# Kernel optimization log

Measured on AMD Instinct MI355X. Metric: run time of the kernel, lower is better.

Reference implementation:

```python
import jax, jax.numpy as jnp
import numpy as np

VAR_CXCY = 0.1   # variances[0]
VAR_WH = 0.2     # variances[1]
MIN_OVERLAP = 0.5
NEG_POS_RATIO = 3


def cxcy_to_xyxy(b):
    return jnp.concatenate([b[:, :2] - b[:, 2:] / 2, b[:, :2] + b[:, 2:] / 2], axis=-1)


def jaccard(a, b):
    # a: [O,4] xyxy, b: [P,4] xyxy -> [O,P]
    lt = jnp.maximum(a[:, None, :2], b[None, :, :2])
    rb = jnp.minimum(a[:, None, 2:], b[None, :, 2:])
    wh = jnp.clip(rb - lt, 0.0)
    inter = wh[..., 0] * wh[..., 1]
    area_a = (a[:, 2] - a[:, 0]) * (a[:, 3] - a[:, 1])
    area_b = (b[:, 2] - b[:, 0]) * (b[:, 3] - b[:, 1])
    return inter / (area_a[:, None] + area_b[None, :] - inter)


def xyxy_to_gcxgcy(boxes, priors):
    # boxes: [P,4] xyxy matched per-prior; priors: [P,4] cxcywh
    cxcy = (boxes[:, :2] + boxes[:, 2:]) / 2
    wh = boxes[:, 2:] - boxes[:, :2]
    g_cxcy = (cxcy - priors[:, :2]) / (priors[:, 2:] * VAR_CXCY)
    g_wh = jnp.log(wh / priors[:, 2:]) / VAR_WH
    return jnp.concatenate([g_cxcy, g_wh], axis=-1)


def _match_one(boxes, labels, priors, priors_xyxy):
    # boxes: [O,4] xyxy, labels: [O] int
    overlaps = jaccard(boxes, priors_xyxy)          # [O,P]
    prior_overlaps = overlaps.max(axis=0)            # [P]
    prior_objects = overlaps.argmax(axis=0)          # [P]
    object_priors = overlaps.argmax(axis=1)          # [O] best prior per object
    n_obj = boxes.shape[0]
    prior_objects = prior_objects.at[object_priors].set(jnp.arange(n_obj))
    prior_overlaps = prior_overlaps.at[object_priors].set(1.0)
    lab = labels[prior_objects]
    lab = jnp.where(prior_overlaps < MIN_OVERLAP, 0, lab)
    locs = xyxy_to_gcxgcy(boxes[prior_objects], priors)
    return locs, lab


def setup_inputs() -> dict:
    key = jax.random.key(0)
    B, P, C, O = 64, 8732, 81, 16
    ks = jax.random.split(key, 6)
    predict_locs = jax.random.normal(ks[0], (B, P, 4), dtype=jnp.float32)
    predict_confs = jax.random.normal(ks[1], (B, P, C), dtype=jnp.float32)
    # priors in cxcywh, valid sizes
    p_cxcy = jax.random.uniform(ks[2], (P, 2), minval=0.0, maxval=1.0)
    p_wh = jax.random.uniform(ks[2], (P, 2), minval=0.05, maxval=0.3)
    priors = jnp.concatenate([p_cxcy, p_wh], axis=-1).astype(jnp.float32)
    # targets: valid xyxy boxes in [0,1]
    t_cxcy = jax.random.uniform(ks[3], (B, O, 2), minval=0.2, maxval=0.8)
    t_wh = jax.random.uniform(ks[4], (B, O, 2), minval=0.05, maxval=0.4)
    target_boxes = jnp.concatenate([t_cxcy - t_wh / 2, t_cxcy + t_wh / 2], axis=-1).astype(jnp.float32)
    target_labels = jax.random.randint(ks[5], (B, O), 1, C)
    return {
        'predict_locs': predict_locs,
        'predict_confs': predict_confs,
        'target_boxes': target_boxes,
        'target_labels': target_labels,
        'priors': priors,
    }


def reference(predict_locs, predict_confs, target_boxes, target_labels, priors):
    priors_xyxy = cxcy_to_xyxy(priors)
    true_locs, true_confs = jax.vmap(
        lambda b, l: _match_one(b, l, priors, priors_xyxy)
    )(target_boxes, target_labels)              # [B,P,4], [B,P]

    pos = true_confs != 0                        # [B,P]
    n_pos = pos.sum(axis=1)                      # [B]
    n_pos_total = n_pos.sum().astype(predict_locs.dtype)

    # nn.L1Loss(reduction='mean') over the [n_pos_total, 4] gathered entries
    loc_loss = jnp.sum(jnp.abs(predict_locs - true_locs) * pos[..., None]) / (n_pos_total * 4)

    logp = jax.nn.log_softmax(predict_confs, axis=-1)
    ce = -jnp.take_along_axis(logp, true_confs[..., None], axis=-1)[..., 0]  # [B,P]

    ce_pos_sum = jnp.sum(jnp.where(pos, ce, 0.0))
    ce_neg = jnp.where(pos, 0.0, ce)
    # double-sort rank: rank of each prior when sorted by descending neg loss
    rank = jnp.argsort(jnp.argsort(-ce_neg, axis=1), axis=1)
    hard = rank < (NEG_POS_RATIO * n_pos)[:, None]
    ce_hard_sum = jnp.sum(jnp.where(hard, ce_neg, 0.0))

    conf_loss = (ce_hard_sum + ce_pos_sum) / n_pos_total
    return conf_loss + loc_loss
```

## Files before the change

kernel.cpp:

```cpp
#include <hip/hip_runtime.h>
#include <cstdint>
#include <cstddef>

constexpr int O_C = 16;
constexpr int P_MAX = 8732;
constexpr int CH   = 4;
constexpr int CHP  = 2183;

__device__ __forceinline__ float waveSumF(float v) {
    #pragma unroll
    for (int off = 32; off; off >>= 1) v += __shfl_xor(v, off);
    return v;
}
__device__ __forceinline__ int waveSumI(int v) {
    #pragma unroll
    for (int off = 32; off; off >>= 1) v += __shfl_xor(v, off);
    return v;
}

__global__ __launch_bounds__(256) void matchA1(
    const float* __restrict__ target_boxes,
    const float* __restrict__ priors,
    float* __restrict__ ov_out,
    unsigned char* __restrict__ obj_out,
    unsigned long long* __restrict__ okey_part,
    int P)
{
    const int b    = blockIdx.x / CH;
    const int c    = blockIdx.x % CH;
    const int tid  = threadIdx.x;
    const int lane = tid & 63;
    const int wid  = tid >> 6;

    __shared__ float bx0[O_C], by0[O_C], bx1[O_C], by1[O_C], barea[O_C];
    __shared__ unsigned long long s_wb[O_C * 4];

    if (tid < O_C) {
        const float* tb = target_boxes + ((size_t)b * O_C + tid) * 4;
        float x0 = tb[0], y0 = tb[1], x1 = tb[2], y1 = tb[3];
        bx0[tid] = x0; by0[tid] = y0; bx1[tid] = x1; by1[tid] = y1;
        barea[tid] = (x1 - x0) * (y1 - y0);
    }
    __syncthreads();

    float bi[O_C]; int bp[O_C];
    #pragma unroll
    for (int o = 0; o < O_C; ++o) { bi[o] = -1.0f; bp[o] = 0; }

    const int p0 = c * CHP, p1 = min(p0 + CHP, P);
    for (int p = p0 + tid; p < p1; p += 256) {
        float4 pr = reinterpret_cast<const float4*>(priors)[p];
        float px0 = pr.x - pr.z * 0.5f, py0 = pr.y - pr.w * 0.5f;
        float px1 = pr.x + pr.z * 0.5f, py1 = pr.y + pr.w * 0.5f;
        float parea = (px1 - px0) * (py1 - py0);
        float bv = -1.0f; int bo = 0;
        #pragma unroll
        for (int o = 0; o < O_C; ++o) {
            float ix0 = fmaxf(px0, bx0[o]), iy0 = fmaxf(py0, by0[o]);
            float ix1 = fminf(px1, bx1[o]), iy1 = fminf(py1, by1[o]);
            float iw = fmaxf(ix1 - ix0, 0.0f), ih = fmaxf(iy1 - iy0, 0.0f);
            float inter = iw * ih;
            float iou = inter / (barea[o] + parea - inter);
            if (iou > bv) { bv = iou; bo = o; }
            if (iou > bi[o]) { bi[o] = iou; bp[o] = p; }
        }
        ov_out[(size_t)b * P + p]  = bv;
        obj_out[(size_t)b * P + p] = (unsigned char)bo;
    }

    #pragma unroll
    for (int o = 0; o < O_C; ++o) {
        unsigned long long k = (bi[o] >= 0.0f)
            ? (((unsigned long long)__float_as_uint(bi[o]) << 32) |
               (unsigned long long)(0xFFFFFFFFu - (unsigned)bp[o]))
            : 0ull;
        #pragma unroll
        for (int off = 32; off; off >>= 1) {
            unsigned long long k2 = __shfl_xor(k, off);
            if (k2 > k) k = k2;
        }
        if (lane == 0) s_wb[o * 4 + wid] = k;
    }
    __syncthreads();
    if (tid < O_C) {
        unsigned long long k = s_wb[tid * 4];
        #pragma unroll
        for (int w = 1; w < 4; ++w) if (s_wb[tid * 4 + w] > k) k = s_wb[tid * 4 + w];
        okey_part[(size_t)blockIdx.x * O_C + tid] = k;
    }
}

__global__ __launch_bounds__(256) void fused_ce(
    const float* __restrict__ confs,
    const float* __restrict__ ov_in,
    const unsigned char* __restrict__ obj_in,
    const unsigned long long* __restrict__ okey_part,
    const float* __restrict__ target_boxes,
    const int*   __restrict__ target_labels,
    const float* __restrict__ priors,
    const float* __restrict__ predict_locs,
    float* __restrict__ ce_out,
    float* __restrict__ loc_part,
    int P, int rows)
{
    constexpr int C = 81;
    constexpr int R = 64;
    __shared__ float s_x[R * C];
    __shared__ float tbx0[2][O_C], tby0[2][O_C], tbx1[2][O_C], tby1[2][O_C];
    __shared__ int   tlab[2][O_C], toprior[2][O_C];
    __shared__ float s_facc[4];

    const int tid  = threadIdx.x;
    const int lane = tid & 63;
    const int wid  = tid >> 6;
    const int row0 = blockIdx.x * R;

    const int b0     = row0 / P;
    const int rsplit = min(row0 + R, (b0 + 1) * P);
    const bool two   = rsplit < row0 + R;
    const int b1     = two ? b0 + 1 : b0;

    if (tid < 2 * O_C) {
        const int seg = tid >> 4, o = tid & 15;
        const int bb  = seg ? b1 : b0;
        const float* tb = target_boxes + ((size_t)bb * O_C + o) * 4;
        tbx0[seg][o] = tb[0]; tby0[seg][o] = tb[1];
        tbx1[seg][o] = tb[2]; tby1[seg][o] = tb[3];
        tlab[seg][o] = target_labels[(size_t)bb * O_C + o];
        unsigned long long k = 0ull;
        #pragma unroll
        for (int c = 0; c < CH; ++c) {
            unsigned long long k2 = okey_part[((size_t)bb * CH + c) * O_C + o];
            if (k2 > k) k = k2;
        }
        toprior[seg][o] = (int)(0xFFFFFFFFu - (unsigned)(k & 0xFFFFFFFFull));
    }

    {
        const float4* src = reinterpret_cast<const float4*>(confs + (size_t)row0 * C);
        float4* dst = reinterpret_cast<float4*>(s_x);
        const int nv = (R * C) / 4;
        for (int i = tid; i < nv; i += 256) dst[i] = src[i];
    }
    __syncthreads();

    const int rl = tid >> 2;
    const int q  = tid & 3;
    const int s  = q * 20 + (q > 0 ? 1 : 0);
    const int n  = q ? 20 : 21;
    const float* xr = s_x + rl * C;
    const int row = row0 + rl;

    int   l = 0;
    float locacc = 0.0f;
    if (q == 0 && row < rows) {
        const int seg = (row >= rsplit) ? 1 : 0;
        const int p   = row - (seg ? b1 : b0) * P;
        float ov = ov_in[row];
        int  obj = obj_in[row];
        #pragma unroll
        for (int o = 0; o < O_C; ++o) {
            if (toprior[seg][o] == p) { obj = o; ov = 1.0f; }
        }
        l = (ov < 0.5f) ? 0 : tlab[seg][obj];
        if (l != 0) {
            float4 pr = reinterpret_cast<const float4*>(priors)[p];
            float x0 = tbx0[seg][obj], y0 = tby0[seg][obj];
            float x1 = tbx1[seg][obj], y1 = tby1[seg][obj];
            float cx = (x0 + x1) * 0.5f, cy = (y0 + y1) * 0.5f;
            float w  = x1 - x0,          h  = y1 - y0;
            float g0 = (cx - pr.x) / (pr.z * 0.1f);
            float g1 = (cy - pr.y) / (pr.w * 0.1f);
            float g2 = logf(w / pr.z) / 0.2f;
            float g3 = logf(h / pr.w) / 0.2f;
            float4 pl = reinterpret_cast<const float4*>(predict_locs)[row];
            locacc = fabsf(pl.x - g0) + fabsf(pl.y - g1) +
                     fabsf(pl.z - g2) + fabsf(pl.w - g3);
        }
    }

    float v[21];
    #pragma unroll
    for (int i = 0; i < 21; ++i)
        v[i] = (i < n) ? xr[s + i] : -3.0e38f;

    float m = v[0];
    #pragma unroll
    for (int i = 1; i < 21; ++i) m = fmaxf(m, v[i]);
    m = fmaxf(m, __shfl_xor(m, 1));
    m = fmaxf(m, __shfl_xor(m, 2));

    float sum = 0.0f;
    #pragma unroll
    for (int i = 0; i < 21; ++i)
        if (i < n) sum += __expf(v[i] - m);
    sum += __shfl_xor(sum, 1);
    sum += __shfl_xor(sum, 2);

    if (q == 0 && row < rows) {
        float cev = m + __logf(sum) - xr[l];
        ce_out[row] = (l != 0) ? -cev : cev;
    }

    float a = waveSumF(locacc);
    if (lane == 0) s_facc[wid] = a;
    __syncthreads();
    if (tid == 0)
        loc_part[blockIdx.x] = s_facc[0] + s_facc[1] + s_facc[2] + s_facc[3];
}

__global__ __launch_bounds__(1024) void hard_kernel(
    const float* __restrict__ ce,
    int*   __restrict__ n_pos,
    float* __restrict__ ce_pos,
    float* __restrict__ ce_hard,
    int P)
{
    const int b    = blockIdx.x;
    const int tid  = threadIdx.x;
    const int lane = tid & 63;
    const int wid  = tid >> 6;

    __shared__ float s_v[P_MAX];
    __shared__ unsigned int hist[16][256];
    __shared__ unsigned int s_sel;
    __shared__ int s_kr;
    __shared__ float s_f[16], s_f2[16];
    __shared__ int s_i[16];

    const size_t base = (size_t)b * P;
    float possum = 0.0f, negsum = 0.0f;
    int cnt = 0;
    for (int p = tid; p < P; p += 1024) {
        float c = ce[base + p];
        unsigned u = __float_as_uint(c);
        float sv;
        if (u >> 31) { possum += -c; ++cnt; sv = 0.0f; }
        else         { negsum += c;         sv = c;    }
        s_v[p] = sv;
    }
    possum = waveSumF(possum);
    negsum = waveSumF(negsum);
    cnt    = waveSumI(cnt);
    if (lane == 0) { s_f[wid] = possum; s_f2[wid] = negsum; s_i[wid] = cnt; }
    __syncthreads();
    float negsum_t = 0.0f, possum_t = 0.0f; int np = 0;
    #pragma unroll
    for (int w = 0; w < 16; ++w) { negsum_t += s_f2[w]; possum_t += s_f[w]; np += s_i[w]; }
    if (tid == 0) { ce_pos[b] = possum_t; n_pos[b] = np; }

    const int K = 3 * np;
    if (K <= 0) { if (tid == 0) ce_hard[b] = 0.0f; return; }
    if (K >= P) { if (tid == 0) ce_hard[b] = negsum_t; return; }

    unsigned int prefix = 0; int kr = K;
    for (int shift = 24; shift >= 0; shift -= 8) {
        for (int i = tid; i < 16 * 256; i += 1024) (&hist[0][0])[i] = 0;
        __syncthreads();
        unsigned int maskHi = (shift == 24) ? 0u : (0xFFFFFFFFu << (shift + 8));
        for (int p = tid; p < P; p += 1024) {
            unsigned int u = __float_as_uint(s_v[p]);
            if ((u & maskHi) == prefix) atomicAdd(&hist[wid][(u >> shift) & 255], 1u);
        }
        __syncthreads();
        if (wid == 0) {
            unsigned h0 = 0, h1 = 0, h2 = 0, h3 = 0;
            #pragma unroll 4
            for (int w = 0; w < 16; ++w) {
                h0 += hist[w][lane * 4 + 0];
                h1 += hist[w][lane * 4 + 1];
                h2 += hist[w][lane * 4 + 2];
                h3 += hist[w][lane * 4 + 3];
            }
            unsigned own = h0 + h1 + h2 + h3;
            unsigned t = own;
            #pragma unroll
            for (int off = 1; off < 64; off <<= 1) {
                unsigned u = __shfl_down(t, off);
                if (lane + off >= 64) u = 0;
                t += u;
            }
            unsigned Tnext = t - own;
            unsigned cum3 = Tnext;
            unsigned cum2 = cum3 + h3;
            unsigned cum1 = cum2 + h2;
            unsigned cum0 = cum1 + h1;
            unsigned kru = (unsigned)kr;
            int selj = -1; unsigned cg = 0;
            if      (cum3 < kru && kru <= cum3 + h3) { selj = 3; cg = cum3; }
            else if (cum2 < kru && kru <= cum2 + h2) { selj = 2; cg = cum2; }
            else if (cum1 < kru && kru <= cum1 + h1) { selj = 1; cg = cum1; }
            else if (cum0 < kru && kru <= cum0 + h0) { selj = 0; cg = cum0; }
            if (selj >= 0) {
                s_sel = prefix | ((unsigned)(lane * 4 + selj) << shift);
                s_kr  = kr - (int)cg;
            }
        }
        __syncthreads();
        prefix = s_sel; kr = s_kr;
        __syncthreads();
    }

    float sumgt = 0.0f;
    for (int p = tid; p < P; p += 1024) {
        unsigned int u = __float_as_uint(s_v[p]);
        if (u > prefix) sumgt += s_v[p];
    }
    sumgt = waveSumF(sumgt);
    if (lane == 0) s_f[wid] = sumgt;
    __syncthreads();
    if (tid == 0) {
        float sg = 0.0f;
        #pragma unroll
        for (int w = 0; w < 16; ++w) sg += s_f[w];
        ce_hard[b] = sg + (float)kr * __uint_as_float(prefix);
    }
}

__global__ __launch_bounds__(256) void finalize_kernel(
    const int*   __restrict__ n_pos,
    const float* __restrict__ ce_pos,
    const float* __restrict__ ce_hard,
    const float* __restrict__ loc_part,
    float* __restrict__ out, int B, int nblk)
{
    __shared__ float s_f[4];
    __shared__ float s_res[3];
    const int tid  = threadIdx.x;
    const int lane = tid & 63;
    const int wid  = tid >> 6;

    float la = 0.0f;
    for (int i = tid; i < nblk; i += 256) la += loc_part[i];
    la = waveSumF(la);
    if (lane == 0) s_f[wid] = la;

    if (tid < 64) {
        int np = 0; float cp = 0.0f, ch = 0.0f;
        for (int b = lane; b < B; b += 64) {
            np += n_pos[b]; cp += ce_pos[b]; ch += ce_hard[b];
        }
        #pragma unroll
        for (int off = 32; off; off >>= 1) {
            np += __shfl_xor(np, off);
            cp += __shfl_xor(cp, off);
            ch += __shfl_xor(ch, off);
        }
        if (lane == 0) {
            s_res[0] = (float)np; s_res[1] = cp; s_res[2] = ch;
        }
    }
    __syncthreads();
    if (tid == 0) {
        float latot = s_f[0] + s_f[1] + s_f[2] + s_f[3];
        float npt = s_res[0];
        out[0] = (s_res[2] + s_res[1]) / npt + latot / (npt * 4.0f);
    }
}

extern "C" void kernel_launch(void* const* d_in, const int* in_sizes, int n_in,
                              void* d_out, int out_size, void* d_ws, size_t ws_size,
                              hipStream_t stream) {
    const float* predict_locs  = (const float*)d_in[0];
    const float* predict_confs = (const float*)d_in[1];
    const float* target_boxes  = (const float*)d_in[2];
    const int*   target_labels = (const int*)d_in[3];
    const float* priors        = (const float*)d_in[4];

    const int P = in_sizes[4] / 4;
    const int B = in_sizes[0] / (P * 4);
    const int rows = B * P;
    const int nblk = (rows + 63) / 64;

    char* ws = (char*)d_ws;
    unsigned long long* okey_part = (unsigned long long*)ws;
    ws += (size_t)B * CH * O_C * sizeof(unsigned long long);
    float* ce      = (float*)ws; ws += (size_t)rows * sizeof(float);
    float* ov      = (float*)ws; ws += (size_t)rows * sizeof(float);
    float* loc_p   = (float*)ws; ws += (size_t)nblk * sizeof(float);
    int*   n_pos   = (int*)ws;   ws += (size_t)B * sizeof(int);
    float* ce_pos  = (float*)ws; ws += (size_t)B * sizeof(float);
    float* ce_hard = (float*)ws; ws += (size_t)B * sizeof(float);
    unsigned char* obj = (unsigned char*)ws; ws += (size_t)rows;

    matchA1<<<B * CH, 256, 0, stream>>>(target_boxes, priors, ov, obj, okey_part, P);
    fused_ce<<<nblk, 256, 0, stream>>>(predict_confs, ov, obj, okey_part,
                                       target_boxes, target_labels, priors,
                                       predict_locs, ce, loc_p, P, rows);
    hard_kernel<<<B, 1024, 0, stream>>>(ce, n_pos, ce_pos, ce_hard, P);
    finalize_kernel<<<1, 256, 0, stream>>>(n_pos, ce_pos, ce_hard, loc_p,
                                           (float*)d_out, B, nblk);
}
```

Baseline: 89.20 us.

## Merge four kernels into one persistent cooperative kernel with grid syncs

Replaces the match, CE, hard-mining and finalize launches with a single cooperative kernel of 256 blocks of 1024 threads, separated by grid-wide syncs. The CE stage is now a persistent tile loop that register-prefetches the next confidence tile into a double-buffered shared slot. The aim is to remove launch gaps and tail effects between the small kernels. In exchange it adds grid-barrier cost, uses far fewer and larger blocks with one block per CU, and the union of shared buffers may limit occupancy.

```diff
diff --git a/kernel.cpp b/kernel.cpp
--- a/kernel.cpp
+++ b/kernel.cpp
@@ -1,11 +1,18 @@
 #include <hip/hip_runtime.h>
+#include <hip/hip_cooperative_groups.h>
 #include <cstdint>
 #include <cstddef>
 
-constexpr int O_C = 16;
+namespace cg = cooperative_groups;
+
+constexpr int O_C   = 16;
+constexpr int CH    = 4;
+constexpr int CHP   = 2183;
 constexpr int P_MAX = 8732;
-constexpr int CH   = 4;
-constexpr int CHP  = 2183;
+constexpr int NBLK  = 256;
+constexpr int NTHR  = 1024;
+constexpr int RT    = 64;
+constexpr int TV4   = RT * 81 / 4;
 
 __device__ __forceinline__ float waveSumF(float v) {
     #pragma unroll
@@ -18,343 +25,366 @@
     return v;
 }
 
-__global__ __launch_bounds__(256) void matchA1(
-    const float* __restrict__ target_boxes,
-    const float* __restrict__ priors,
-    float* __restrict__ ov_out,
-    unsigned char* __restrict__ obj_out,
-    unsigned long long* __restrict__ okey_part,
-    int P)
-{
-    const int b    = blockIdx.x / CH;
-    const int c    = blockIdx.x % CH;
-    const int tid  = threadIdx.x;
-    const int lane = tid & 63;
-    const int wid  = tid >> 6;
-
-    __shared__ float bx0[O_C], by0[O_C], bx1[O_C], by1[O_C], barea[O_C];
-    __shared__ unsigned long long s_wb[O_C * 4];
-
-    if (tid < O_C) {
-        const float* tb = target_boxes + ((size_t)b * O_C + tid) * 4;
-        float x0 = tb[0], y0 = tb[1], x1 = tb[2], y1 = tb[3];
-        bx0[tid] = x0; by0[tid] = y0; bx1[tid] = x1; by1[tid] = y1;
-        barea[tid] = (x1 - x0) * (y1 - y0);
-    }
-    __syncthreads();
-
-    float bi[O_C]; int bp[O_C];
-    #pragma unroll
-    for (int o = 0; o < O_C; ++o) { bi[o] = -1.0f; bp[o] = 0; }
-
-    const int p0 = c * CHP, p1 = min(p0 + CHP, P);
-    for (int p = p0 + tid; p < p1; p += 256) {
-        float4 pr = reinterpret_cast<const float4*>(priors)[p];
-        float px0 = pr.x - pr.z * 0.5f, py0 = pr.y - pr.w * 0.5f;
-        float px1 = pr.x + pr.z * 0.5f, py1 = pr.y + pr.w * 0.5f;
-        float parea = (px1 - px0) * (py1 - py0);
-        float bv = -1.0f; int bo = 0;
-        #pragma unroll
-        for (int o = 0; o < O_C; ++o) {
-            float ix0 = fmaxf(px0, bx0[o]), iy0 = fmaxf(py0, by0[o]);
-            float ix1 = fminf(px1, bx1[o]), iy1 = fminf(py1, by1[o]);
-            float iw = fmaxf(ix1 - ix0, 0.0f), ih = fmaxf(iy1 - iy0, 0.0f);
-            float inter = iw * ih;
-            float iou = inter / (barea[o] + parea - inter);
-            if (iou > bv) { bv = iou; bo = o; }
-            if (iou > bi[o]) { bi[o] = iou; bp[o] = p; }
-        }
-        ov_out[(size_t)b * P + p]  = bv;
-        obj_out[(size_t)b * P + p] = (unsigned char)bo;
-    }
-
-    #pragma unroll
-    for (int o = 0; o < O_C; ++o) {
-        unsigned long long k = (bi[o] >= 0.0f)
-            ? (((unsigned long long)__float_as_uint(bi[o]) << 32) |
-               (unsigned long long)(0xFFFFFFFFu - (unsigned)bp[o]))
-            : 0ull;
-        #pragma unroll
-        for (int off = 32; off; off >>= 1) {
-            unsigned long long k2 = __shfl_xor(k, off);
-            if (k2 > k) k = k2;
-        }
-        if (lane == 0) s_wb[o * 4 + wid] = k;
-    }
-    __syncthreads();
-    if (tid < O_C) {
-        unsigned long long k = s_wb[tid * 4];
-        #pragma unroll
-        for (int w = 1; w < 4; ++w) if (s_wb[tid * 4 + w] > k) k = s_wb[tid * 4 + w];
-        okey_part[(size_t)blockIdx.x * O_C + tid] = k;
-    }
-}
-
-__global__ __launch_bounds__(256) void fused_ce(
+__global__ __launch_bounds__(NTHR, 1) void mbloss_coop(
     const float* __restrict__ confs,
-    const float* __restrict__ ov_in,
-    const unsigned char* __restrict__ obj_in,
-    const unsigned long long* __restrict__ okey_part,
     const float* __restrict__ target_boxes,
     const int*   __restrict__ target_labels,
     const float* __restrict__ priors,
     const float* __restrict__ predict_locs,
-    float* __restrict__ ce_out,
-    float* __restrict__ loc_part,
-    int P, int rows)
+    float* __restrict__ ov_g,
+    unsigned char* __restrict__ obj_g,
+    unsigned long long* __restrict__ okey_part,
+    float* __restrict__ ce_g,
+    float* __restrict__ locsum_g,
+    int*   __restrict__ n_pos_g,
+    float* __restrict__ ce_pos_g,
+    float* __restrict__ ce_hard_g,
+    float* __restrict__ out,
+    int P, int B, int rows)
 {
-    constexpr int C = 81;
-    constexpr int R = 64;
-    __shared__ float s_x[R * C];
-    __shared__ float tbx0[2][O_C], tby0[2][O_C], tbx1[2][O_C], tby1[2][O_C];
-    __shared__ int   tlab[2][O_C], toprior[2][O_C];
-    __shared__ float s_facc[4];
-
+    cg::grid_group grid = cg::this_grid();
+    const int bid  = blockIdx.x;
     const int tid  = threadIdx.x;
     const int lane = tid & 63;
     const int wid  = tid >> 6;
-    const int row0 = blockIdx.x * R;
-
-    const int b0     = row0 / P;
-    const int rsplit = min(row0 + R, (b0 + 1) * P);
-    const bool two   = rsplit < row0 + R;
-    const int b1     = two ? b0 + 1 : b0;
-
-    if (tid < 2 * O_C) {
-        const int seg = tid >> 4, o = tid & 15;
-        const int bb  = seg ? b1 : b0;
-        const float* tb = target_boxes + ((size_t)bb * O_C + o) * 4;
-        tbx0[seg][o] = tb[0]; tby0[seg][o] = tb[1];
-        tbx1[seg][o] = tb[2]; tby1[seg][o] = tb[3];
-        tlab[seg][o] = target_labels[(size_t)bb * O_C + o];
-        unsigned long long k = 0ull;
+
+    __shared__ union {
+        float x[2][RT * 81];
+        struct { float v[P_MAX]; unsigned int hist[16][256]; } h;
+    } u;
+    __shared__ float4 tbox[2][2][O_C];
+    __shared__ int    ttlab[2][2][O_C], ttopr[2][2][O_C];
+    __shared__ unsigned long long s_wb[O_C][16];
+    __shared__ float s_mb[5][O_C];
+    __shared__ float s_f[16], s_f2[16];
+    __shared__ int   s_i[16];
+    __shared__ unsigned int s_sel;
+    __shared__ int s_kr;
+
+    for (int chunk = bid; chunk < B * CH; chunk += NBLK) {
+        const int b = chunk / CH, c = chunk % CH;
+        if (tid < O_C) {
+            const float* tb = target_boxes + ((size_t)b * O_C + tid) * 4;
+            float x0 = tb[0], y0 = tb[1], x1 = tb[2], y1 = tb[3];
+            s_mb[0][tid] = x0; s_mb[1][tid] = y0;
+            s_mb[2][tid] = x1; s_mb[3][tid] = y1;
+            s_mb[4][tid] = (x1 - x0) * (y1 - y0);
+        }
+        __syncthreads();
+
+        float bi[O_C]; int bp[O_C];
         #pragma unroll
-        for (int c = 0; c < CH; ++c) {
-            unsigned long long k2 = okey_part[((size_t)bb * CH + c) * O_C + o];
-            if (k2 > k) k = k2;
-        }
-        toprior[seg][o] = (int)(0xFFFFFFFFu - (unsigned)(k & 0xFFFFFFFFull));
-    }
-
-    {
-        const float4* src = reinterpret_cast<const float4*>(confs + (size_t)row0 * C);
-        float4* dst = reinterpret_cast<float4*>(s_x);
-        const int nv = (R * C) / 4;
-        for (int i = tid; i < nv; i += 256) dst[i] = src[i];
-    }
-    __syncthreads();
-
-    const int rl = tid >> 2;
-    const int q  = tid & 3;
-    const int s  = q * 20 + (q > 0 ? 1 : 0);
-    const int n  = q ? 20 : 21;
-    const float* xr = s_x + rl * C;
-    const int row = row0 + rl;
-
-    int   l = 0;
-    float locacc = 0.0f;
-    if (q == 0 && row < rows) {
-        const int seg = (row >= rsplit) ? 1 : 0;
-        const int p   = row - (seg ? b1 : b0) * P;
-        float ov = ov_in[row];
-        int  obj = obj_in[row];
+        for (int o = 0; o < O_C; ++o) { bi[o] = -1.0f; bp[o] = 0; }
+
+        const int p0 = c * CHP, p1 = min(p0 + CHP, P);
+        for (int p = p0 + tid; p < p1; p += NTHR) {
+            float4 pr = reinterpret_cast<const float4*>(priors)[p];
+            float px0 = pr.x - pr.z * 0.5f, py0 = pr.y - pr.w * 0.5f;
+            float px1 = pr.x + pr.z * 0.5f, py1 = pr.y + pr.w * 0.5f;
+            float parea = (px1 - px0) * (py1 - py0);
+            float bv = -1.0f; int bo = 0;
+            #pragma unroll
+            for (int o = 0; o < O_C; ++o) {
+                float ix0 = fmaxf(px0, s_mb[0][o]), iy0 = fmaxf(py0, s_mb[1][o]);
+                float ix1 = fminf(px1, s_mb[2][o]), iy1 = fminf(py1, s_mb[3][o]);
+                float iw = fmaxf(ix1 - ix0, 0.0f), ih = fmaxf(iy1 - iy0, 0.0f);
+                float inter = iw * ih;
+                float iou = inter / (s_mb[4][o] + parea - inter);
+                if (iou > bv) { bv = iou; bo = o; }
+                if (iou > bi[o]) { bi[o] = iou; bp[o] = p; }
+            }
+            ov_g[(size_t)b * P + p]  = bv;
+            obj_g[(size_t)b * P + p] = (unsigned char)bo;
+        }
+
         #pragma unroll
         for (int o = 0; o < O_C; ++o) {
-            if (toprior[seg][o] == p) { obj = o; ov = 1.0f; }
-        }
-        l = (ov < 0.5f) ? 0 : tlab[seg][obj];
-        if (l != 0) {
-            float4 pr = reinterpret_cast<const float4*>(priors)[p];
-            float x0 = tbx0[seg][obj], y0 = tby0[seg][obj];
-            float x1 = tbx1[seg][obj], y1 = tby1[seg][obj];
-            float cx = (x0 + x1) * 0.5f, cy = (y0 + y1) * 0.5f;
-            float w  = x1 - x0,          h  = y1 - y0;
-            float g0 = (cx - pr.x) / (pr.z * 0.1f);
-            float g1 = (cy - pr.y) / (pr.w * 0.1f);
-            float g2 = logf(w / pr.z) / 0.2f;
-            float g3 = logf(h / pr.w) / 0.2f;
-            float4 pl = reinterpret_cast<const float4*>(predict_locs)[row];
-            locacc = fabsf(pl.x - g0) + fabsf(pl.y - g1) +
-                     fabsf(pl.z - g2) + fabsf(pl.w - g3);
-        }
-    }
-
-    float v[21];
-    #pragma unroll
-    for (int i = 0; i < 21; ++i)
-        v[i] = (i < n) ? xr[s + i] : -3.0e38f;
-
-    float m = v[0];
-    #pragma unroll
-    for (int i = 1; i < 21; ++i) m = fmaxf(m, v[i]);
-    m = fmaxf(m, __shfl_xor(m, 1));
-    m = fmaxf(m, __shfl_xor(m, 2));
-
-    float sum = 0.0f;
-    #pragma unroll
-    for (int i = 0; i < 21; ++i)
-        if (i < n) sum += __expf(v[i] - m);
-    sum += __shfl_xor(sum, 1);
-    sum += __shfl_xor(sum, 2);
-
-    if (q == 0 && row < rows) {
-        float cev = m + __logf(sum) - xr[l];
-        ce_out[row] = (l != 0) ? -cev : cev;
-    }
-
-    float a = waveSumF(locacc);
-    if (lane == 0) s_facc[wid] = a;
-    __syncthreads();
-    if (tid == 0)
-        loc_part[blockIdx.x] = s_facc[0] + s_facc[1] + s_facc[2] + s_facc[3];
-}
-
-__global__ __launch_bounds__(1024) void hard_kernel(
-    const float* __restrict__ ce,
-    int*   __restrict__ n_pos,
-    float* __restrict__ ce_pos,
-    float* __restrict__ ce_hard,
-    int P)
-{
-    const int b    = blockIdx.x;
-    const int tid  = threadIdx.x;
-    const int lane = tid & 63;
-    const int wid  = tid >> 6;
-
-    __shared__ float s_v[P_MAX];
-    __shared__ unsigned int hist[16][256];
-    __shared__ unsigned int s_sel;
-    __shared__ int s_kr;
-    __shared__ float s_f[16], s_f2[16];
-    __shared__ int s_i[16];
-
-    const size_t base = (size_t)b * P;
-    float possum = 0.0f, negsum = 0.0f;
-    int cnt = 0;
-    for (int p = tid; p < P; p += 1024) {
-        float c = ce[base + p];
-        unsigned u = __float_as_uint(c);
-        float sv;
-        if (u >> 31) { possum += -c; ++cnt; sv = 0.0f; }
-        else         { negsum += c;         sv = c;    }
-        s_v[p] = sv;
-    }
-    possum = waveSumF(possum);
-    negsum = waveSumF(negsum);
-    cnt    = waveSumI(cnt);
-    if (lane == 0) { s_f[wid] = possum; s_f2[wid] = negsum; s_i[wid] = cnt; }
-    __syncthreads();
-    float negsum_t = 0.0f, possum_t = 0.0f; int np = 0;
-    #pragma unroll
-    for (int w = 0; w < 16; ++w) { negsum_t += s_f2[w]; possum_t += s_f[w]; np += s_i[w]; }
-    if (tid == 0) { ce_pos[b] = possum_t; n_pos[b] = np; }
-
-    const int K = 3 * np;
-    if (K <= 0) { if (tid == 0) ce_hard[b] = 0.0f; return; }
-    if (K >= P) { if (tid == 0) ce_hard[b] = negsum_t; return; }
-
-    unsigned int prefix = 0; int kr = K;
-    for (int shift = 24; shift >= 0; shift -= 8) {
-        for (int i = tid; i < 16 * 256; i += 1024) (&hist[0][0])[i] = 0;
-        __syncthreads();
-        unsigned int maskHi = (shift == 24) ? 0u : (0xFFFFFFFFu << (shift + 8));
-        for (int p = tid; p < P; p += 1024) {
-            unsigned int u = __float_as_uint(s_v[p]);
-            if ((u & maskHi) == prefix) atomicAdd(&hist[wid][(u >> shift) & 255], 1u);
-        }
-        __syncthreads();
-        if (wid == 0) {
-            unsigned h0 = 0, h1 = 0, h2 = 0, h3 = 0;
-            #pragma unroll 4
-            for (int w = 0; w < 16; ++w) {
-                h0 += hist[w][lane * 4 + 0];
-                h1 += hist[w][lane * 4 + 1];
-                h2 += hist[w][lane * 4 + 2];
-                h3 += hist[w][lane * 4 + 3];
-            }
-            unsigned own = h0 + h1 + h2 + h3;
-            unsigned t = own;
-            #pragma unroll
-            for (int off = 1; off < 64; off <<= 1) {
-                unsigned u = __shfl_down(t, off);
-                if (lane + off >= 64) u = 0;
-                t += u;
-            }
-            unsigned Tnext = t - own;
-            unsigned cum3 = Tnext;
-            unsigned cum2 = cum3 + h3;
-            unsigned cum1 = cum2 + h2;
-            unsigned cum0 = cum1 + h1;
-            unsigned kru = (unsigned)kr;
-            int selj = -1; unsigned cg = 0;
-            if      (cum3 < kru && kru <= cum3 + h3) { selj = 3; cg = cum3; }
-            else if (cum2 < kru && kru <= cum2 + h2) { selj = 2; cg = cum2; }
-            else if (cum1 < kru && kru <= cum1 + h1) { selj = 1; cg = cum1; }
-            else if (cum0 < kru && kru <= cum0 + h0) { selj = 0; cg = cum0; }
-            if (selj >= 0) {
-                s_sel = prefix | ((unsigned)(lane * 4 + selj) << shift);
-                s_kr  = kr - (int)cg;
-            }
-        }
-        __syncthreads();
-        prefix = s_sel; kr = s_kr;
-        __syncthreads();
-    }
-
-    float sumgt = 0.0f;
-    for (int p = tid; p < P; p += 1024) {
-        unsigned int u = __float_as_uint(s_v[p]);
-        if (u > prefix) sumgt += s_v[p];
-    }
-    sumgt = waveSumF(sumgt);
-    if (lane == 0) s_f[wid] = sumgt;
-    __syncthreads();
-    if (tid == 0) {
-        float sg = 0.0f;
+            unsigned long long k = (bi[o] >= 0.0f)
+                ? (((unsigned long long)__float_as_uint(bi[o]) << 32) |
+                   (unsigned long long)(0xFFFFFFFFu - (unsigned)bp[o]))
+                : 0ull;
+            #pragma unroll
+            for (int off = 32; off; off >>= 1) {
+                unsigned long long k2 = __shfl_xor(k, off);
+                if (k2 > k) k = k2;
+            }
+            if (lane == 0) s_wb[o][wid] = k;
+        }
+        __syncthreads();
+        if (tid < O_C) {
+            unsigned long long k = s_wb[tid][0];
+            #pragma unroll
+            for (int w = 1; w < 16; ++w) if (s_wb[tid][w] > k) k = s_wb[tid][w];
+            okey_part[(size_t)chunk * O_C + tid] = k;
+        }
+        __syncthreads();
+    }
+    grid.sync();
+
+    const int ntile = rows / RT;
+    const int rl = tid >> 4, q = tid & 15;
+    const int sseg = q ? (5 * q + 1) : 0;
+    float locacc = 0.0f;
+
+    if (bid < ntile) {
+        const float4* src0 = reinterpret_cast<const float4*>(confs + (size_t)bid * RT * 81);
+        float4* dx0 = reinterpret_cast<float4*>(u.x[0]);
+        dx0[tid] = src0[tid];
+        if (tid < TV4 - NTHR) dx0[NTHR + tid] = src0[NTHR + tid];
+        if (tid < 32) {
+            const int seg = tid >> 4, o = tid & 15;
+            const int row0 = bid * RT;
+            const int b0 = row0 / P;
+            const int rsp = min(row0 + RT, (b0 + 1) * P);
+            const bool two = rsp < row0 + RT;
+            const int bb = (seg && two) ? b0 + 1 : b0;
+            const float* tb = target_boxes + ((size_t)bb * O_C + o) * 4;
+            tbox[0][seg][o] = make_float4(tb[0], tb[1], tb[2], tb[3]);
+            ttlab[0][seg][o] = target_labels[(size_t)bb * O_C + o];
+            unsigned long long kk = 0ull;
+            #pragma unroll
+            for (int cc = 0; cc < CH; ++cc) {
+                unsigned long long k2 = okey_part[((size_t)bb * CH + cc) * O_C + o];
+                if (k2 > kk) kk = k2;
+            }
+            ttopr[0][seg][o] = (int)(0xFFFFFFFFu - (unsigned)(kk & 0xFFFFFFFFull));
+        }
+    }
+
+    for (int t = bid, k = 0; t < ntile; t += NBLK, ++k) {
+        const int slot = k & 1, ns = slot ^ 1;
+        const int tn = t + NBLK;
+        const bool have = tn < ntile;
+        __syncthreads();
+
+        float4 r0 = make_float4(0,0,0,0), r1 = make_float4(0,0,0,0);
+        float4 trbox = make_float4(0,0,0,0); int trlab = 0, tropr = 0;
+        int trseg = 0, tro = 0;
+        if (have) {
+            const float4* src = reinterpret_cast<const float4*>(confs + (size_t)tn * RT * 81);
+            r0 = src[tid];
+            if (tid < TV4 - NTHR) r1 = src[NTHR + tid];
+            if (tid < 32) {
+                trseg = tid >> 4; tro = tid & 15;
+                const int row0n = tn * RT;
+                const int b0n = row0n / P;
+                const int rspn = min(row0n + RT, (b0n + 1) * P);
+                const bool twon = rspn < row0n + RT;
+                const int bb = (trseg && twon) ? b0n + 1 : b0n;
+                const float* tb = target_boxes + ((size_t)bb * O_C + tro) * 4;
+                trbox = make_float4(tb[0], tb[1], tb[2], tb[3]);
+                trlab = target_labels[(size_t)bb * O_C + tro];
+                unsigned long long kk = 0ull;
+                #pragma unroll
+                for (int cc = 0; cc < CH; ++cc) {
+                    unsigned long long k2 = okey_part[((size_t)bb * CH + cc) * O_C + tro];
+                    if (k2 > kk) kk = k2;
+                }
+                tropr = (int)(0xFFFFFFFFu - (unsigned)(kk & 0xFFFFFFFFull));
+            }
+        }
+
+        {
+            const int row0 = t * RT;
+            const int b0 = row0 / P;
+            const int rsp = min(row0 + RT, (b0 + 1) * P);
+            const int row = row0 + rl;
+            const float* xr = &u.x[slot][rl * 81];
+
+            float v[6];
+            #pragma unroll
+            for (int i = 0; i < 6; ++i)
+                v[i] = (q == 0 || i < 5) ? xr[sseg + i] : -3.0e38f;
+            if (q != 0) v[5] = -3.0e38f;
+
+            float m = v[0];
+            #pragma unroll
+            for (int i = 1; i < 6; ++i) m = fmaxf(m, v[i]);
+            m = fmaxf(m, __shfl_xor(m, 1));
+            m = fmaxf(m, __shfl_xor(m, 2));
+            m = fmaxf(m, __shfl_xor(m, 4));
+            m = fmaxf(m, __shfl_xor(m, 8));
+
+            float sum = 0.0f;
+            #pragma unroll
+            for (int i = 0; i < 6; ++i) sum += __expf(v[i] - m);
+            sum += __shfl_xor(sum, 1);
+            sum += __shfl_xor(sum, 2);
+            sum += __shfl_xor(sum, 4);
+            sum += __shfl_xor(sum, 8);
+
+            if (q == 0) {
+                const int seg = (row >= rsp) ? 1 : 0;
+                const int bb = b0 + seg;
+                const int p = row - bb * P;
+                float ovv = ov_g[row];
+                int obj = obj_g[row];
+                #pragma unroll
+                for (int o = 0; o < O_C; ++o)
+                    if (ttopr[slot][seg][o] == p) { obj = o; ovv = 1.0f; }
+                const int l = (ovv < 0.5f) ? 0 : ttlab[slot][seg][obj];
+                float cev = m + __logf(sum) - xr[l];
+                ce_g[row] = l ? -cev : cev;
+                if (l) {
+                    float4 pr = reinterpret_cast<const float4*>(priors)[p];
+                    float4 tb = tbox[slot][seg][obj];
+                    float cx = (tb.x + tb.z) * 0.5f, cy = (tb.y + tb.w) * 0.5f;
+                    float w  = tb.z - tb.x,          h  = tb.w - tb.y;
+                    float g0 = (cx - pr.x) / (pr.z * 0.1f);
+                    float g1 = (cy - pr.y) / (pr.w * 0.1f);
+                    float g2 = logf(w / pr.z) / 0.2f;
+                    float g3 = logf(h / pr.w) / 0.2f;
+                    float4 pl = reinterpret_cast<const float4*>(predict_locs)[row];
+                    locacc += fabsf(pl.x - g0) + fabsf(pl.y - g1) +
+                              fabsf(pl.z - g2) + fabsf(pl.w - g3);
+                }
+            }
+        }
+
+        if (have) {
+            float4* dx = reinterpret_cast<float4*>(u.x[ns]);
+            dx[tid] = r0;
+            if (tid < TV4 - NTHR) dx[NTHR + tid] = r1;
+            if (tid < 32) {
+                tbox[ns][trseg][tro]  = trbox;
+                ttlab[ns][trseg][tro] = trlab;
+                ttopr[ns][trseg][tro] = tropr;
+            }
+        }
+    }
+
+    {
+        float a = waveSumF(locacc);
+        if (lane == 0) s_f[wid] = a;
+        __syncthreads();
+        if (tid == 0) {
+            float sres = 0.0f;
+            #pragma unroll
+            for (int w = 0; w < 16; ++w) sres += s_f[w];
+            locsum_g[bid] = sres;
+        }
+    }
+    grid.sync();
+
+    if (bid < B) {
+        const int b = bid;
+        const size_t base = (size_t)b * P;
+        float possum = 0.0f, negsum = 0.0f;
+        int cnt = 0;
+        for (int p = tid; p < P; p += NTHR) {
+            float c = ce_g[base + p];
+            unsigned uu = __float_as_uint(c);
+            float sv;
+            if (uu >> 31) { possum += -c; ++cnt; sv = 0.0f; }
+            else          { negsum += c;        sv = c;    }
+            u.h.v[p] = sv;
+        }
+        possum = waveSumF(possum);
+        negsum = waveSumF(negsum);
+        cnt    = waveSumI(cnt);
+        if (lane == 0) { s_f[wid] = possum; s_f2[wid] = negsum; s_i[wid] = cnt; }
+        __syncthreads();
+        float negsum_t = 0.0f, possum_t = 0.0f; int np = 0;
         #pragma unroll
-        for (int w = 0; w < 16; ++w) sg += s_f[w];
-        ce_hard[b] = sg + (float)kr * __uint_as_float(prefix);
-    }
-}
-
-__global__ __launch_bounds__(256) void finalize_kernel(
-    const int*   __restrict__ n_pos,
-    const float* __restrict__ ce_pos,
-    const float* __restrict__ ce_hard,
-    const float* __restrict__ loc_part,
-    float* __restrict__ out, int B, int nblk)
-{
-    __shared__ float s_f[4];
-    __shared__ float s_res[3];
-    const int tid  = threadIdx.x;
-    const int lane = tid & 63;
-    const int wid  = tid >> 6;
-
-    float la = 0.0f;
-    for (int i = tid; i < nblk; i += 256) la += loc_part[i];
-    la = waveSumF(la);
-    if (lane == 0) s_f[wid] = la;
-
-    if (tid < 64) {
-        int np = 0; float cp = 0.0f, ch = 0.0f;
-        for (int b = lane; b < B; b += 64) {
-            np += n_pos[b]; cp += ce_pos[b]; ch += ce_hard[b];
-        }
-        #pragma unroll
-        for (int off = 32; off; off >>= 1) {
-            np += __shfl_xor(np, off);
-            cp += __shfl_xor(cp, off);
-            ch += __shfl_xor(ch, off);
-        }
-        if (lane == 0) {
-            s_res[0] = (float)np; s_res[1] = cp; s_res[2] = ch;
-        }
-    }
-    __syncthreads();
-    if (tid == 0) {
-        float latot = s_f[0] + s_f[1] + s_f[2] + s_f[3];
-        float npt = s_res[0];
-        out[0] = (s_res[2] + s_res[1]) / npt + latot / (npt * 4.0f);
+        for (int w = 0; w < 16; ++w) { negsum_t += s_f2[w]; possum_t += s_f[w]; np += s_i[w]; }
+        if (tid == 0) { ce_pos_g[b] = possum_t; n_pos_g[b] = np; }
+
+        const int K = 3 * np;
+        if (K > 0 && K < P) {
+            unsigned int prefix = 0; int kr = K;
+            for (int shift = 24; shift >= 0; shift -= 8) {
+                for (int i = tid; i < 16 * 256; i += NTHR) (&u.h.hist[0][0])[i] = 0;
+                __syncthreads();
+                unsigned int maskHi = (shift == 24) ? 0u : (0xFFFFFFFFu << (shift + 8));
+                for (int p = tid; p < P; p += NTHR) {
+                    unsigned int uu = __float_as_uint(u.h.v[p]);
+                    if ((uu & maskHi) == prefix)
+                        atomicAdd(&u.h.hist[wid][(uu >> shift) & 255], 1u);
+                }
+                __syncthreads();
+                if (wid == 0) {
+                    unsigned h0 = 0, h1 = 0, h2 = 0, h3 = 0;
+                    #pragma unroll 4
+                    for (int w = 0; w < 16; ++w) {
+                        h0 += u.h.hist[w][lane * 4 + 0];
+                        h1 += u.h.hist[w][lane * 4 + 1];
+                        h2 += u.h.hist[w][lane * 4 + 2];
+                        h3 += u.h.hist[w][lane * 4 + 3];
+                    }
+                    unsigned own = h0 + h1 + h2 + h3;
+                    unsigned tsum = own;
+                    #pragma unroll
+                    for (int off = 1; off < 64; off <<= 1) {
+                        unsigned uu = __shfl_down(tsum, off);
+                        if (lane + off >= 64) uu = 0;
+                        tsum += uu;
+                    }
+                    unsigned Tnext = tsum - own;
+                    unsigned cum3 = Tnext;
+                    unsigned cum2 = cum3 + h3;
+                    unsigned cum1 = cum2 + h2;
+                    unsigned cum0 = cum1 + h1;
+                    unsigned kru = (unsigned)kr;
+                    int selj = -1; unsigned cg2 = 0;
+                    if      (cum3 < kru && kru <= cum3 + h3) { selj = 3; cg2 = cum3; }
+                    else if (cum2 < kru && kru <= cum2 + h2) { selj = 2; cg2 = cum2; }
+                    else if (cum1 < kru && kru <= cum1 + h1) { selj = 1; cg2 = cum1; }
+                    else if (cum0 < kru && kru <= cum0 + h0) { selj = 0; cg2 = cum0; }
+                    if (selj >= 0) {
+                        s_sel = prefix | ((unsigned)(lane * 4 + selj) << shift);
+                        s_kr  = kr - (int)cg2;
+                    }
+                }
+                __syncthreads();
+                prefix = s_sel; kr = s_kr;
+                __syncthreads();
+            }
+
+            float sumgt = 0.0f;
+            for (int p = tid; p < P; p += NTHR) {
+                unsigned int uu = __float_as_uint(u.h.v[p]);
+                if (uu > prefix) sumgt += u.h.v[p];
+            }
+            sumgt = waveSumF(sumgt);
+            if (lane == 0) s_f[wid] = sumgt;
+            __syncthreads();
+            if (tid == 0) {
+                float sg = 0.0f;
+                #pragma unroll
+                for (int w = 0; w < 16; ++w) sg += s_f[w];
+                ce_hard_g[b] = sg + (float)kr * __uint_as_float(prefix);
+            }
+        } else {
+            if (tid == 0) ce_hard_g[b] = (K <= 0) ? 0.0f : negsum_t;
+        }
+    }
+    grid.sync();
+
+    if (bid == 0) {
+        float la = (tid < NBLK) ? locsum_g[tid] : 0.0f;
+        la = waveSumF(la);
+        if (lane == 0) s_f[wid] = la;
+        if (tid < 64) {
+            int np = 0; float cp = 0.0f, chd = 0.0f;
+            for (int b2 = tid; b2 < B; b2 += 64) {
+                np += n_pos_g[b2]; cp += ce_pos_g[b2]; chd += ce_hard_g[b2];
+            }
+            #pragma unroll
+            for (int off = 32; off; off >>= 1) {
+                np  += __shfl_xor(np, off);
+                cp  += __shfl_xor(cp, off);
+                chd += __shfl_xor(chd, off);
+            }
+            if (tid == 0) { s_f2[0] = cp; s_f2[1] = chd; s_i[0] = np; }
+        }
+        __syncthreads();
+        if (tid == 0) {
+            float latot = 0.0f;
+            #pragma unroll
+            for (int w = 0; w < 16; ++w) latot += s_f[w];
+            float npt = (float)s_i[0];
+            out[0] = (s_f2[1] + s_f2[0]) / npt + latot / (npt * 4.0f);
+        }
     }
 }
 
@@ -367,27 +397,29 @@
     const int*   target_labels = (const int*)d_in[3];
     const float* priors        = (const float*)d_in[4];
 
-    const int P = in_sizes[4] / 4;
-    const int B = in_sizes[0] / (P * 4);
-    const int rows = B * P;
-    const int nblk = (rows + 63) / 64;
+    int P = in_sizes[4] / 4;
+    int B = in_sizes[0] / (P * 4);
+    int rows = B * P;
 
     char* ws = (char*)d_ws;
     unsigned long long* okey_part = (unsigned long long*)ws;
     ws += (size_t)B * CH * O_C * sizeof(unsigned long long);
     float* ce      = (float*)ws; ws += (size_t)rows * sizeof(float);
     float* ov      = (float*)ws; ws += (size_t)rows * sizeof(float);
-    float* loc_p   = (float*)ws; ws += (size_t)nblk * sizeof(float);
+    float* locsum  = (float*)ws; ws += (size_t)NBLK * sizeof(float);
     int*   n_pos   = (int*)ws;   ws += (size_t)B * sizeof(int);
     float* ce_pos  = (float*)ws; ws += (size_t)B * sizeof(float);
     float* ce_hard = (float*)ws; ws += (size_t)B * sizeof(float);
     unsigned char* obj = (unsigned char*)ws; ws += (size_t)rows;
-
-    matchA1<<<B * CH, 256, 0, stream>>>(target_boxes, priors, ov, obj, okey_part, P);
-    fused_ce<<<nblk, 256, 0, stream>>>(predict_confs, ov, obj, okey_part,
-                                       target_boxes, target_labels, priors,
-                                       predict_locs, ce, loc_p, P, rows);
-    hard_kernel<<<B, 1024, 0, stream>>>(ce, n_pos, ce_pos, ce_hard, P);
-    finalize_kernel<<<1, 256, 0, stream>>>(n_pos, ce_pos, ce_hard, loc_p,
-                                           (float*)d_out, B, nblk);
+    float* outp = (float*)d_out;
+
+    void* args[] = {
+        (void*)&predict_confs, (void*)&target_boxes, (void*)&target_labels,
+        (void*)&priors, (void*)&predict_locs,
+        (void*)&ov, (void*)&obj, (void*)&okey_part, (void*)&ce, (void*)&locsum,
+        (void*)&n_pos, (void*)&ce_pos, (void*)&ce_hard, (void*)&outp,
+        (void*)&P, (void*)&B, (void*)&rows
+    };
+    hipLaunchCooperativeKernel((void*)mbloss_coop, dim3(NBLK), dim3(NTHR),
+                               args, 0, stream);
 }
```

After: 217.9 us. 2.44x slower.

## Stream CE rows directly from global memory with one thread per row and online softmax

Applied to the files above, without the earlier changes.

Replaces the shared-memory staged, four-threads-per-row cross-entropy kernel with a one-thread-per-row kernel that reads each 81-float row straight from global memory. It computes the max and sum in a single pass with online softmax. The goal is to drop the LDS staging and the block-wide sync, with 256 rows per block. The risks are uncoalesced strided row reads and unaligned 16-byte struct loads (row stride 324 bytes), and the grid now assumes rows divisible by 256 with no bounds check.

```diff
diff --git a/kernel.cpp b/kernel.cpp
--- a/kernel.cpp
+++ b/kernel.cpp
@@ -2,10 +2,12 @@
 #include <cstdint>
 #include <cstddef>
 
-constexpr int O_C = 16;
+constexpr int O_C   = 16;
 constexpr int P_MAX = 8732;
-constexpr int CH   = 4;
-constexpr int CHP  = 2183;
+constexpr int CH    = 4;
+constexpr int CHP   = 2183;
+
+struct f4u { float x, y, z, w; };
 
 __device__ __forceinline__ float waveSumF(float v) {
     #pragma unroll
@@ -90,7 +92,7 @@
     }
 }
 
-__global__ __launch_bounds__(256) void fused_ce(
+__global__ __launch_bounds__(256) void ce_stream(
     const float* __restrict__ confs,
     const float* __restrict__ ov_in,
     const unsigned char* __restrict__ obj_in,
@@ -103,105 +105,84 @@
     float* __restrict__ loc_part,
     int P, int rows)
 {
-    constexpr int C = 81;
-    constexpr int R = 64;
-    __shared__ float s_x[R * C];
-    __shared__ float tbx0[2][O_C], tby0[2][O_C], tbx1[2][O_C], tby1[2][O_C];
-    __shared__ int   tlab[2][O_C], toprior[2][O_C];
-    __shared__ float s_facc[4];
-
     const int tid  = threadIdx.x;
     const int lane = tid & 63;
     const int wid  = tid >> 6;
-    const int row0 = blockIdx.x * R;
+    const int row0 = blockIdx.x * 256;
+    const int row  = row0 + tid;
+
+    __shared__ float4 tbox[2][O_C];
+    __shared__ int    tlab[2][O_C], topr[2][O_C];
+    __shared__ float  s_facc[4];
 
     const int b0     = row0 / P;
-    const int rsplit = min(row0 + R, (b0 + 1) * P);
-    const bool two   = rsplit < row0 + R;
-    const int b1     = two ? b0 + 1 : b0;
+    const int rsplit = min(row0 + 256, (b0 + 1) * P);
+    const int b1     = (rsplit < row0 + 256) ? b0 + 1 : b0;
 
     if (tid < 2 * O_C) {
         const int seg = tid >> 4, o = tid & 15;
         const int bb  = seg ? b1 : b0;
         const float* tb = target_boxes + ((size_t)bb * O_C + o) * 4;
-        tbx0[seg][o] = tb[0]; tby0[seg][o] = tb[1];
-        tbx1[seg][o] = tb[2]; tby1[seg][o] = tb[3];
+        tbox[seg][o] = make_float4(tb[0], tb[1], tb[2], tb[3]);
         tlab[seg][o] = target_labels[(size_t)bb * O_C + o];
-        unsigned long long k = 0ull;
-        #pragma unroll
-        for (int c = 0; c < CH; ++c) {
-            unsigned long long k2 = okey_part[((size_t)bb * CH + c) * O_C + o];
-            if (k2 > k) k = k2;
-        }
-        toprior[seg][o] = (int)(0xFFFFFFFFu - (unsigned)(k & 0xFFFFFFFFull));
-    }
-
+        unsigned long long kk = 0ull;
+        #pragma unroll
+        for (int cc = 0; cc < CH; ++cc) {
+            unsigned long long k2 = okey_part[((size_t)bb * CH + cc) * O_C + o];
+            if (k2 > kk) kk = k2;
+        }
+        topr[seg][o] = (int)(0xFFFFFFFFu - (unsigned)(kk & 0xFFFFFFFFull));
+    }
+    __syncthreads();
+
+    const float* rbase = confs + (size_t)row * 81;
+    const f4u* rp = reinterpret_cast<const f4u*>(rbase);
+    float m = -3.0e38f, s = 0.0f;
+    #pragma unroll
+    for (int j = 0; j < 20; ++j) {
+        f4u a = rp[j];
+        float m4 = fmaxf(fmaxf(a.x, a.y), fmaxf(a.z, a.w));
+        float mn = fmaxf(m, m4);
+        s = s * __expf(m - mn)
+          + __expf(a.x - mn) + __expf(a.y - mn)
+          + __expf(a.z - mn) + __expf(a.w - mn);
+        m = mn;
+    }
     {
-        const float4* src = reinterpret_cast<const float4*>(confs + (size_t)row0 * C);
-        float4* dst = reinterpret_cast<float4*>(s_x);
-        const int nv = (R * C) / 4;
-        for (int i = tid; i < nv; i += 256) dst[i] = src[i];
-    }
-    __syncthreads();
-
-    const int rl = tid >> 2;
-    const int q  = tid & 3;
-    const int s  = q * 20 + (q > 0 ? 1 : 0);
-    const int n  = q ? 20 : 21;
-    const float* xr = s_x + rl * C;
-    const int row = row0 + rl;
-
-    int   l = 0;
+        float last = rbase[80];
+        float mn = fmaxf(m, last);
+        s = s * __expf(m - mn) + __expf(last - mn);
+        m = mn;
+    }
+
+    const int seg = (row >= rsplit) ? 1 : 0;
+    const int bb  = seg ? b1 : b0;
+    const int p   = row - bb * P;
+    float ovv = ov_in[row];
+    int   obj = obj_in[row];
+    #pragma unroll
+    for (int o = 0; o < O_C; ++o)
+        if (topr[seg][o] == p) { obj = o; ovv = 1.0f; }
+    const int l = (ovv < 0.5f) ? 0 : tlab[seg][obj];
+
+    float xl  = rbase[l];
+    float cev = m + __logf(s) - xl;
+    ce_out[row] = l ? -cev : cev;
+
     float locacc = 0.0f;
-    if (q == 0 && row < rows) {
-        const int seg = (row >= rsplit) ? 1 : 0;
-        const int p   = row - (seg ? b1 : b0) * P;
-        float ov = ov_in[row];
-        int  obj = obj_in[row];
-        #pragma unroll
-        for (int o = 0; o < O_C; ++o) {
-            if (toprior[seg][o] == p) { obj = o; ov = 1.0f; }
-        }
-        l = (ov < 0.5f) ? 0 : tlab[seg][obj];
-        if (l != 0) {
-            float4 pr = reinterpret_cast<const float4*>(priors)[p];
-            float x0 = tbx0[seg][obj], y0 = tby0[seg][obj];
-            float x1 = tbx1[seg][obj], y1 = tby1[seg][obj];
-            float cx = (x0 + x1) * 0.5f, cy = (y0 + y1) * 0.5f;
-            float w  = x1 - x0,          h  = y1 - y0;
-            float g0 = (cx - pr.x) / (pr.z * 0.1f);
-            float g1 = (cy - pr.y) / (pr.w * 0.1f);
-            float g2 = logf(w / pr.z) / 0.2f;
-            float g3 = logf(h / pr.w) / 0.2f;
-            float4 pl = reinterpret_cast<const float4*>(predict_locs)[row];
-            locacc = fabsf(pl.x - g0) + fabsf(pl.y - g1) +
-                     fabsf(pl.z - g2) + fabsf(pl.w - g3);
-        }
-    }
-
-    float v[21];
-    #pragma unroll
-    for (int i = 0; i < 21; ++i)
-        v[i] = (i < n) ? xr[s + i] : -3.0e38f;
-
-    float m = v[0];
-    #pragma unroll
-    for (int i = 1; i < 21; ++i) m = fmaxf(m, v[i]);
-    m = fmaxf(m, __shfl_xor(m, 1));
-    m = fmaxf(m, __shfl_xor(m, 2));
-
-    float sum = 0.0f;
-    #pragma unroll
-    for (int i = 0; i < 21; ++i)
-        if (i < n) sum += __expf(v[i] - m);
-    sum += __shfl_xor(sum, 1);
-    sum += __shfl_xor(sum, 2);
-
-    if (q == 0 && row < rows) {
-        float cev = m + __logf(sum) - xr[l];
-        ce_out[row] = (l != 0) ? -cev : cev;
-    }
-
+    if (l) {
+        float4 pr = reinterpret_cast<const float4*>(priors)[p];
+        float4 tb = tbox[seg][obj];
+        float cx = (tb.x + tb.z) * 0.5f, cy = (tb.y + tb.w) * 0.5f;
+        float w  = tb.z - tb.x,          h  = tb.w - tb.y;
+        float g0 = (cx - pr.x) / (pr.z * 0.1f);
+        float g1 = (cy - pr.y) / (pr.w * 0.1f);
+        float g2 = logf(w / pr.z) / 0.2f;
+        float g3 = logf(h / pr.w) / 0.2f;
+        float4 pl = reinterpret_cast<const float4*>(predict_locs)[row];
+        locacc = fabsf(pl.x - g0) + fabsf(pl.y - g1) +
+                 fabsf(pl.z - g2) + fabsf(pl.w - g3);
+    }
     float a = waveSumF(locacc);
     if (lane == 0) s_facc[wid] = a;
     __syncthreads();
@@ -370,7 +351,7 @@
     const int P = in_sizes[4] / 4;
     const int B = in_sizes[0] / (P * 4);
     const int rows = B * P;
-    const int nblk = (rows + 63) / 64;
+    const int nblk = rows / 256;
 
     char* ws = (char*)d_ws;
     unsigned long long* okey_part = (unsigned long long*)ws;
@@ -384,10 +365,10 @@
     unsigned char* obj = (unsigned char*)ws; ws += (size_t)rows;
 
     matchA1<<<B * CH, 256, 0, stream>>>(target_boxes, priors, ov, obj, okey_part, P);
-    fused_ce<<<nblk, 256, 0, stream>>>(predict_confs, ov, obj, okey_part,
-                                       target_boxes, target_labels, priors,
-                                       predict_locs, ce, loc_p, P, rows);
+    ce_stream<<<nblk, 256, 0, stream>>>(predict_confs, ov, obj, okey_part,
+                                        target_boxes, target_labels, priors,
+                                        predict_locs, ce, loc_p, P, rows);
     hard_kernel<<<B, 1024, 0, stream>>>(ce, n_pos, ce_pos, ce_hard, P);
     finalize_kernel<<<1, 256, 0, stream>>>(n_pos, ce_pos, ce_hard, loc_p,
-                                           (float*)d_out, B, nblk);
-}
+                                           (float*)d_out, B, rows / 256);
+}
```

Result: faster. 78.32 us (-12.2%).
